# Kernel optimization log

Measured on AMD Instinct MI355X. Metric: run time of the kernel, lower is better.

The kernel has to match this reference:

```python
import jax, jax.numpy as jnp
import numpy as np

B, D, NQ, NK, K = 8, 384, 2048, 2048, 8
NEG_SLOPE = 0.2


def setup_inputs() -> dict:
    key = jax.random.key(0)
    ks = jax.random.split(key, 6)
    return {
        "query_coords": jax.random.normal(ks[0], (B, 3, NQ), jnp.float32),
        "query_features": jax.random.normal(ks[1], (B, D, NQ), jnp.float32),
        "key_coords": jax.random.normal(ks[2], (B, 3, NK), jnp.float32),
        "key_features": jax.random.normal(ks[3], (B, D, NK), jnp.float32),
        "W": jax.random.normal(ks[4], (D, 2 * D), jnp.float32) / np.sqrt(2.0 * D),
        "b": jnp.zeros((D,), jnp.float32),
    }


def _knn_idx(qc, kc, k):
    # qc: [B,3,Nq], kc: [B,3,Nk] -> indices of k nearest keys per query [B,Nq,k]
    q2 = jnp.sum(qc * qc, axis=1)                      # [B,Nq]
    k2 = jnp.sum(kc * kc, axis=1)                      # [B,Nk]
    inner = jnp.einsum('bcq,bck->bqk', qc, kc)         # [B,Nq,Nk]
    dist = q2[:, :, None] - 2.0 * inner + k2[:, None, :]
    _, idx = jax.lax.top_k(-dist, k)
    return idx


def reference(query_coords, query_features, key_coords, key_features, W, b):
    idx = _knn_idx(query_coords, key_coords, K)        # [B,Nq,K]
    kf = jnp.transpose(key_features, (0, 2, 1))        # [B,Nk,D]
    qf = jnp.transpose(query_features, (0, 2, 1))      # [B,Nq,D]
    nbr = jax.vmap(lambda f, i: f[i])(kf, idx)         # gather -> [B,Nq,K,D]
    center = qf[:, :, None, :]                          # [B,Nq,1,D]
    # DGCNN/PoinTr graph feature: concat(neighbor - center, center)
    geom = jnp.concatenate(
        [nbr - center, jnp.broadcast_to(center, nbr.shape)], axis=-1)  # [B,Nq,K,2D]
    h = jnp.einsum('bqkf,df->bqkd', geom, W) + b        # Linear(2D -> D)
    h = jnp.where(h >= 0, h, NEG_SLOPE * h)             # LeakyReLU(0.2)
    return jnp.max(h, axis=2)                           # max over k -> [B,Nq,D]
```

## Files before the change

kernel.cpp:

```cpp
#include <hip/hip_runtime.h>
#include <hip/hip_bf16.h>
#include <float.h>

#define BB 8
#define DD 384
#define NQ 2048
#define NK 2048
#define NEG 0.2f

typedef __attribute__((ext_vector_type(8))) __bf16 bf16x8v;
typedef __attribute__((ext_vector_type(4))) float  float4v;

__device__ __forceinline__ unsigned short bf16_rne(float x) {
  unsigned int u = __float_as_uint(x);
  return (unsigned short)((u + 0x7FFFu + ((u >> 16) & 1u)) >> 16);
}
__device__ __forceinline__ float bf16_to_f32(unsigned short h) {
  return __uint_as_float(((unsigned int)h) << 16);
}

#define QPW 4

__global__ __launch_bounds__(256) void knn_kernel(
    const float* __restrict__ qc, const float* __restrict__ kc,
    int* __restrict__ idx)
{
  __shared__ float4 ksm[NK];
  const int b = blockIdx.y;
  const int t = threadIdx.x;
  const float* kcb = kc + (size_t)b * 3 * NK;
  for (int i = t; i < NK; i += 256) {
    float x = kcb[i], y = kcb[NK + i], z = kcb[2 * NK + i];
    ksm[i] = make_float4(x, y, z, (x * x + y * y) + z * z);
  }
  __syncthreads();

  const int w = t >> 6, l = t & 63;
  const float* qcb = qc + (size_t)b * 3 * NQ;

  for (int qi = 0; qi < QPW; ++qi) {
    const int q = blockIdx.x * (4 * QPW) + w * QPW + qi;
    const float qx = qcb[q], qy = qcb[NQ + q], qz = qcb[2 * NQ + q];
    const float q2 = (qx * qx + qy * qy) + qz * qz;

    float d[32];
    #pragma unroll
    for (int j = 0; j < 32; ++j) {
      float4 kv = ksm[j * 64 + l];
      float inner = (qx * kv.x + qy * kv.y) + qz * kv.z;
      d[j] = (q2 - 2.0f * inner) + kv.w;
    }

    int outk[8];
    #pragma unroll
    for (int r = 0; r < 8; ++r) {
      float m = d[0]; int mj = 0;
      #pragma unroll
      for (int j = 1; j < 32; ++j) {
        bool c = d[j] < m;
        m  = c ? d[j] : m;
        mj = c ? j : mj;
      }
      int mkey = mj * 64 + l;
      #pragma unroll
      for (int off = 32; off >= 1; off >>= 1) {
        float om = __shfl_xor(m, off);
        int   ok = __shfl_xor(mkey, off);
        bool take = (om < m) || (om == m && ok < mkey);
        m    = take ? om : m;
        mkey = take ? ok : mkey;
      }
      outk[r] = mkey;
      const bool mine = (l == (mkey & 63));
      const int  slot = mkey >> 6;
      #pragma unroll
      for (int j = 0; j < 32; ++j) {
        bool kill = mine && (j == slot);
        d[j] = kill ? FLT_MAX : d[j];
      }
    }
    int myv = outk[0];
    #pragma unroll
    for (int r = 1; r < 8; ++r) myv = (l == r) ? outk[r] : myv;
    if (l < 8) idx[((size_t)b * NQ + q) * 8 + l] = myv;
  }
}

__global__ __launch_bounds__(256) void transpose_pack_kernel(
    const float* __restrict__ kf, const float* __restrict__ qf,
    unsigned short* __restrict__ Apk)
{
  __shared__ float tile[64][68];
  const int t = threadIdx.x;
  const int z = blockIdx.z;
  const int b = z & 7;
  const float* src = ((z >> 3) ? qf : kf) + (size_t)b * DD * 2048;
  const int f0 = blockIdx.y * 64;
  const int n0 = blockIdx.x * 64;

  {
    const int fr = t >> 2, nc = (t & 3) * 16;
    const float* p = src + (size_t)(f0 + fr) * 2048 + n0 + nc;
    float4 v0 = *(const float4*)(p);
    float4 v1 = *(const float4*)(p + 4);
    float4 v2 = *(const float4*)(p + 8);
    float4 v3 = *(const float4*)(p + 12);
    *(float4*)&tile[fr][nc]      = v0;
    *(float4*)&tile[fr][nc + 4]  = v1;
    *(float4*)&tile[fr][nc + 8]  = v2;
    *(float4*)&tile[fr][nc + 12] = v3;
  }
  __syncthreads();
  {
    const int nr = t >> 2, fc = (t & 3) * 16;
    unsigned int hp[8], lp[8];
    #pragma unroll
    for (int i = 0; i < 8; ++i) {
      float va = tile[fc + 2 * i][nr];
      float vb = tile[fc + 2 * i + 1][nr];
      unsigned short ha = bf16_rne(va), hb = bf16_rne(vb);
      unsigned short la = bf16_rne(va - bf16_to_f32(ha));
      unsigned short lb = bf16_rne(vb - bf16_to_f32(hb));
      hp[i] = (unsigned int)ha | ((unsigned int)hb << 16);
      lp[i] = (unsigned int)la | ((unsigned int)lb << 16);
    }
    unsigned short* row = Apk + ((size_t)z * 2048 + n0 + nr) * (2 * DD);
    *(uint4*)(row + f0 + fc)          = make_uint4(hp[0], hp[1], hp[2], hp[3]);
    *(uint4*)(row + f0 + fc + 8)      = make_uint4(hp[4], hp[5], hp[6], hp[7]);
    *(uint4*)(row + DD + f0 + fc)     = make_uint4(lp[0], lp[1], lp[2], lp[3]);
    *(uint4*)(row + DD + f0 + fc + 8) = make_uint4(lp[4], lp[5], lp[6], lp[7]);
  }
}

__global__ __launch_bounds__(192) void wpack_kernel(
    const float* __restrict__ W, unsigned short* __restrict__ Wpk)
{
  const int d = blockIdx.x;
  const int mode = blockIdx.y;
  const int t = threadIdx.x;
  const float* wrow = W + (size_t)d * (2 * DD) + t * 2;
  float2 w1 = *(const float2*)(wrow);
  float a = w1.x, c = w1.y;
  if (mode) {
    float2 w2 = *(const float2*)(wrow + DD);
    a = w2.x - a; c = w2.y - c;
  }
  unsigned short ha = bf16_rne(a), hc = bf16_rne(c);
  unsigned short la = bf16_rne(a - bf16_to_f32(ha));
  unsigned short lc = bf16_rne(c - bf16_to_f32(hc));
  unsigned short* orow = Wpk + ((size_t)mode * DD + d) * (2 * DD);
  *(unsigned int*)(orow + t * 2)      = (unsigned int)ha | ((unsigned int)hc << 16);
  *(unsigned int*)(orow + DD + t * 2) = (unsigned int)la | ((unsigned int)lc << 16);
}

__global__ __launch_bounds__(256) void proj_gemm_mfma(
    const unsigned short* __restrict__ Apk,
    const unsigned short* __restrict__ Wpk,
    const float* __restrict__ bias,
    float* __restrict__ pk, float* __restrict__ pq)
{
  __shared__ unsigned short Alds[128][72];
  __shared__ unsigned short Blds[128][72];

  const int t = threadIdx.x;
  const int z = blockIdx.z, b = z & 7, mode = z >> 3;
  const int n0 = blockIdx.x * 128;
  const int d0 = blockIdx.y * 128;
  const int w = t >> 6, l = t & 63;
  const int wn = w & 1, wd = w >> 1;
  const int lr = l & 15, g = l >> 4;

  float4v acc[4][4];
  #pragma unroll
  for (int i = 0; i < 4; ++i)
    #pragma unroll
    for (int j = 0; j < 4; ++j) acc[i][j] = (float4v){0.f, 0.f, 0.f, 0.f};

  const int sr = t >> 1, sh = (t & 1) * 32;
  const unsigned short* asrc = Apk + ((size_t)z * 2048 + n0 + sr) * (2 * DD) + (t & 1) * DD;
  const unsigned short* bsrc = Wpk + ((size_t)mode * DD + d0 + sr) * (2 * DD) + (t & 1) * DD;

  for (int ks = 0; ks < 12; ++ks) {
    const int kt = ks * 32;
    float4 a0 = *(const float4*)(asrc + kt);
    float4 a1 = *(const float4*)(asrc + kt + 8);
    float4 a2 = *(const float4*)(asrc + kt + 16);
    float4 a3 = *(const float4*)(asrc + kt + 24);
    float4 b0 = *(const float4*)(bsrc + kt);
    float4 b1 = *(const float4*)(bsrc + kt + 8);
    float4 b2 = *(const float4*)(bsrc + kt + 16);
    float4 b3 = *(const float4*)(bsrc + kt + 24);
    __syncthreads();
    *(float4*)&Alds[sr][sh]      = a0;
    *(float4*)&Alds[sr][sh + 8]  = a1;
    *(float4*)&Alds[sr][sh + 16] = a2;
    *(float4*)&Alds[sr][sh + 24] = a3;
    *(float4*)&Blds[sr][sh]      = b0;
    *(float4*)&Blds[sr][sh + 8]  = b1;
    *(float4*)&Blds[sr][sh + 16] = b2;
    *(float4*)&Blds[sr][sh + 24] = b3;
    __syncthreads();

    bf16x8v ah[4], al[4], bh[4], bl[4];
    #pragma unroll
    for (int i = 0; i < 4; ++i) {
      ah[i] = *(const bf16x8v*)&Alds[wn * 64 + i * 16 + lr][g * 8];
      al[i] = *(const bf16x8v*)&Alds[wn * 64 + i * 16 + lr][32 + g * 8];
      bh[i] = *(const bf16x8v*)&Blds[wd * 64 + i * 16 + lr][g * 8];
      bl[i] = *(const bf16x8v*)&Blds[wd * 64 + i * 16 + lr][32 + g * 8];
    }
    #pragma unroll
    for (int i = 0; i < 4; ++i)
      #pragma unroll
      for (int j = 0; j < 4; ++j) {
        acc[i][j] = __builtin_amdgcn_mfma_f32_16x16x32_bf16(ah[i], bh[j], acc[i][j], 0, 0, 0);
        acc[i][j] = __builtin_amdgcn_mfma_f32_16x16x32_bf16(ah[i], bl[j], acc[i][j], 0, 0, 0);
        acc[i][j] = __builtin_amdgcn_mfma_f32_16x16x32_bf16(al[i], bh[j], acc[i][j], 0, 0, 0);
      }
  }

  float bv[4];
  #pragma unroll
  for (int j = 0; j < 4; ++j)
    bv[j] = mode ? bias[d0 + wd * 64 + j * 16 + lr] : 0.f;

  float* out = (mode ? pq : pk) + (size_t)b * 2048 * DD;
  #pragma unroll
  for (int i = 0; i < 4; ++i) {
    const int nb_ = n0 + wn * 64 + i * 16 + g * 4;
    #pragma unroll
    for (int j = 0; j < 4; ++j) {
      const int dcol = d0 + wd * 64 + j * 16 + lr;
      #pragma unroll
      for (int r = 0; r < 4; ++r)
        out[(size_t)(nb_ + r) * DD + dcol] = acc[i][j][r] + bv[j];
    }
  }
}

__global__ __launch_bounds__(256) void proj_gemm_all(
    const float* __restrict__ kf, const float* __restrict__ qf,
    const float* __restrict__ W, const float* __restrict__ bias,
    float* __restrict__ pk, float* __restrict__ pq)
{
  __shared__ float At[16][128];
  __shared__ float Bt[16][132];
  const int t = threadIdx.x;
  const int z = blockIdx.z, b = z & 7, mode = z >> 3;
  const int n0 = blockIdx.x * 128, d0 = blockIdx.y * 128;
  const int td = t & 15, tn = t >> 4;
  float acc[8][8];
  #pragma unroll
  for (int i = 0; i < 8; ++i)
    #pragma unroll
    for (int j = 0; j < 8; ++j) acc[i][j] = 0.f;
  const float* feats = mode ? qf : kf;
  float* out = mode ? pq : pk;
  const float* fb = feats + (size_t)b * DD * 2048;
  const int ar = t >> 5, ac = (t & 31) * 4, bdl = t >> 2, bf = (t & 3) * 4;
  float4 sa0, sa1, sw1a, sw1b, sw2a, sw2b;
#define PREFETCH(KT)                                                           \
  {                                                                            \
    sa0 = *(const float4*)&fb[(size_t)((KT) + ar) * 2048 + n0 + ac];           \
    sa1 = *(const float4*)&fb[(size_t)((KT) + ar + 8) * 2048 + n0 + ac];       \
    const float* wr0 = W + (size_t)(d0 + bdl) * (2 * DD) + (KT) + bf;          \
    const float* wr1 = W + (size_t)(d0 + bdl + 64) * (2 * DD) + (KT) + bf;     \
    sw1a = *(const float4*)wr0; sw1b = *(const float4*)wr1;                    \
    if (mode) { sw2a = *(const float4*)(wr0 + DD); sw2b = *(const float4*)(wr1 + DD); } \
  }
  PREFETCH(0);
  for (int kt = 0; kt < DD; kt += 16) {
    *(float4*)&At[ar][ac]     = sa0;
    *(float4*)&At[ar + 8][ac] = sa1;
    {
      float4 w = sw1a;
      if (mode) { w.x = sw2a.x - w.x; w.y = sw2a.y - w.y; w.z = sw2a.z - w.z; w.w = sw2a.w - w.w; }
      Bt[bf + 0][bdl] = w.x; Bt[bf + 1][bdl] = w.y; Bt[bf + 2][bdl] = w.z; Bt[bf + 3][bdl] = w.w;
    }
    {
      float4 w = sw1b;
      if (mode) { w.x = sw2b.x - w.x; w.y = sw2b.y - w.y; w.z = sw2b.z - w.z; w.w = sw2b.w - w.w; }
      Bt[bf + 0][bdl + 64] = w.x; Bt[bf + 1][bdl + 64] = w.y; Bt[bf + 2][bdl + 64] = w.z; Bt[bf + 3][bdl + 64] = w.w;
    }
    __syncthreads();
    if (kt + 16 < DD) PREFETCH(kt + 16);
    #pragma unroll
    for (int k = 0; k < 16; ++k) {
      float a[8], bb[8];
      {
        float4 v = *(const float4*)&At[k][tn * 4];
        a[0] = v.x; a[1] = v.y; a[2] = v.z; a[3] = v.w;
        v = *(const float4*)&At[k][tn * 4 + 64];
        a[4] = v.x; a[5] = v.y; a[6] = v.z; a[7] = v.w;
        v = *(const float4*)&Bt[k][td * 4];
        bb[0] = v.x; bb[1] = v.y; bb[2] = v.z; bb[3] = v.w;
        v = *(const float4*)&Bt[k][td * 4 + 64];
        bb[4] = v.x; bb[5] = v.y; bb[6] = v.z; bb[7] = v.w;
      }
      #pragma unroll
      for (int i = 0; i < 8; ++i)
        #pragma unroll
        for (int j = 0; j < 8; ++j)
          acc[i][j] = fmaf(a[i], bb[j], acc[i][j]);
    }
    __syncthreads();
  }
#undef PREFETCH
  float4 blo = make_float4(0.f, 0.f, 0.f, 0.f);
  float4 bhi = make_float4(0.f, 0.f, 0.f, 0.f);
  if (mode) {
    blo = *(const float4*)&bias[d0 + td * 4];
    bhi = *(const float4*)&bias[d0 + td * 4 + 64];
  }
  float* ob = out + (size_t)b * 2048 * DD;
  #pragma unroll
  for (int i = 0; i < 8; ++i) {
    int n = n0 + tn * 4 + (i & 3) + ((i >= 4) ? 64 : 0);
    float4 c0, c1;
    c0.x = acc[i][0] + blo.x; c0.y = acc[i][1] + blo.y;
    c0.z = acc[i][2] + blo.z; c0.w = acc[i][3] + blo.w;
    c1.x = acc[i][4] + bhi.x; c1.y = acc[i][5] + bhi.y;
    c1.z = acc[i][6] + bhi.z; c1.w = acc[i][7] + bhi.w;
    *(float4*)&ob[(size_t)n * DD + d0 + td * 4]      = c0;
    *(float4*)&ob[(size_t)n * DD + d0 + td * 4 + 64] = c1;
  }
}

__global__ __launch_bounds__(384) void gather_max_kernel(
    const float4* __restrict__ pk4, const float4* pq4,
    const int* __restrict__ idx, float4* out4)
{
  const int t = threadIdx.x;
  const int bq0 = blockIdx.x * 4;
  __shared__ int nb[4][8];
  if (t < 32) nb[t >> 3][t & 7] = idx[(size_t)(bq0 + (t >> 3)) * 8 + (t & 7)];
  __syncthreads();
  const int q_l = t / 96;
  const int dv  = t - q_l * 96;
  const int bq  = bq0 + q_l;
  const int b   = bq >> 11;
  const float4* pkb = pk4 + (size_t)b * NK * 96;
  float4 m = make_float4(-FLT_MAX, -FLT_MAX, -FLT_MAX, -FLT_MAX);
  #pragma unroll
  for (int s = 0; s < 8; ++s) {
    float4 v = pkb[(size_t)nb[q_l][s] * 96 + dv];
    m.x = fmaxf(m.x, v.x); m.y = fmaxf(m.y, v.y);
    m.z = fmaxf(m.z, v.z); m.w = fmaxf(m.w, v.w);
  }
  float4 c = pq4[(size_t)bq * 96 + dv];
  float4 r;
  r.x = m.x + c.x; r.y = m.y + c.y; r.z = m.z + c.z; r.w = m.w + c.w;
  r.x = (r.x >= 0.f) ? r.x : NEG * r.x;
  r.y = (r.y >= 0.f) ? r.y : NEG * r.y;
  r.z = (r.z >= 0.f) ? r.z : NEG * r.z;
  r.w = (r.w >= 0.f) ? r.w : NEG * r.w;
  out4[(size_t)bq * 96 + dv] = r;
}

extern "C" void kernel_launch(void* const* d_in, const int* in_sizes, int n_in,
                              void* d_out, int out_size, void* d_ws, size_t ws_size,
                              hipStream_t stream) {
  const float* qc   = (const float*)d_in[0];
  const float* qf   = (const float*)d_in[1];
  const float* kc   = (const float*)d_in[2];
  const float* kf   = (const float*)d_in[3];
  const float* W    = (const float*)d_in[4];
  const float* bias = (const float*)d_in[5];
  float* out = (float*)d_out;
  char* ws = (char*)d_ws;

  const size_t APK_BYTES = (size_t)16 * 2048 * (2 * DD) * 2;
  const size_t WPK_BYTES = (size_t)2 * DD * (2 * DD) * 2;
  const size_t PK_BYTES  = (size_t)BB * NK * DD * 4;
  const size_t IDX_BYTES = (size_t)BB * NQ * 8 * 4;

  if (ws_size >= APK_BYTES + WPK_BYTES + PK_BYTES + IDX_BYTES) {
    unsigned short* Apk = (unsigned short*)ws;
    unsigned short* Wpk = (unsigned short*)(ws + APK_BYTES);
    float* pk = (float*)(ws + APK_BYTES + WPK_BYTES);
    int*   ix = (int*)  (ws + APK_BYTES + WPK_BYTES + PK_BYTES);
    float* pq = out;

    transpose_pack_kernel<<<dim3(32, 6, 16), 256, 0, stream>>>(kf, qf, Apk);
    wpack_kernel<<<dim3(DD, 2), 192, 0, stream>>>(W, Wpk);
    knn_kernel<<<dim3(NQ / (4 * QPW), BB), 256, 0, stream>>>(qc, kc, ix);
    proj_gemm_mfma<<<dim3(16, 3, 16), 256, 0, stream>>>(Apk, Wpk, bias, pk, pq);
    gather_max_kernel<<<dim3(BB * NQ / 4), 384, 0, stream>>>(
        (const float4*)pk, (const float4*)pq, ix, (float4*)out);
  } else {
    float* pk = (float*)ws;
    float* pq = (float*)(ws + PK_BYTES);
    int*   ix = (int*)  (ws + 2 * PK_BYTES);
    knn_kernel<<<dim3(NQ / (4 * QPW), BB), 256, 0, stream>>>(qc, kc, ix);
    proj_gemm_all<<<dim3(16, 3, 16), 256, 0, stream>>>(kf, qf, W, bias, pk, pq);
    gather_max_kernel<<<dim3(BB * NQ / 4), 384, 0, stream>>>(
        (const float4*)pk, (const float4*)pq, ix, (float4*)out);
  }
}
```

Before: 264.4 us.

## Prepack key coords to global and parallelize KNN with tree argmin

```diff
diff --git a/kernel.cpp b/kernel.cpp
--- a/kernel.cpp
+++ b/kernel.cpp
@@ -19,71 +19,96 @@
   return __uint_as_float(((unsigned int)h) << 16);
 }
 
-#define QPW 4
+__global__ __launch_bounds__(256) void kpack_kernel(
+    const float* __restrict__ kc, float4* __restrict__ kpk)
+{
+  const int b = blockIdx.y;
+  const int i = blockIdx.x * 256 + threadIdx.x;
+  const float* kcb = kc + (size_t)b * 3 * NK;
+  float x = kcb[i], y = kcb[NK + i], z = kcb[2 * NK + i];
+  kpk[(size_t)b * NK + i] = make_float4(x, y, z, (x * x + y * y) + z * z);
+}
 
 __global__ __launch_bounds__(256) void knn_kernel(
-    const float* __restrict__ qc, const float* __restrict__ kc,
+    const float* __restrict__ qc, const float4* __restrict__ kpk,
     int* __restrict__ idx)
 {
-  __shared__ float4 ksm[NK];
+  const int t = threadIdx.x;
   const int b = blockIdx.y;
-  const int t = threadIdx.x;
-  const float* kcb = kc + (size_t)b * 3 * NK;
-  for (int i = t; i < NK; i += 256) {
-    float x = kcb[i], y = kcb[NK + i], z = kcb[2 * NK + i];
-    ksm[i] = make_float4(x, y, z, (x * x + y * y) + z * z);
-  }
-  __syncthreads();
-
   const int w = t >> 6, l = t & 63;
+  const int q = blockIdx.x * 4 + w;
+
   const float* qcb = qc + (size_t)b * 3 * NQ;
-
-  for (int qi = 0; qi < QPW; ++qi) {
-    const int q = blockIdx.x * (4 * QPW) + w * QPW + qi;
-    const float qx = qcb[q], qy = qcb[NQ + q], qz = qcb[2 * NQ + q];
-    const float q2 = (qx * qx + qy * qy) + qz * qz;
-
-    float d[32];
+  const float qx = qcb[q], qy = qcb[NQ + q], qz = qcb[2 * NQ + q];
+  const float q2 = (qx * qx + qy * qy) + qz * qz;
+
+  const float4* kb = kpk + (size_t)b * NK;
+  float d[32];
+  #pragma unroll
+  for (int j = 0; j < 32; ++j) {
+    float4 kv = kb[j * 64 + l];
+    float inner = (qx * kv.x + qy * kv.y) + qz * kv.z;
+    d[j] = (q2 - 2.0f * inner) + kv.w;
+  }
+
+  int outk[8];
+  #pragma unroll
+  for (int r = 0; r < 8; ++r) {
+    float v16[16]; int i16[16];
+    #pragma unroll
+    for (int i = 0; i < 16; ++i) {
+      bool c = d[2 * i + 1] < d[2 * i];
+      v16[i] = c ? d[2 * i + 1] : d[2 * i];
+      i16[i] = c ? 2 * i + 1 : 2 * i;
+    }
+    float v8[8]; int i8[8];
+    #pragma unroll
+    for (int i = 0; i < 8; ++i) {
+      bool c = v16[2 * i + 1] < v16[2 * i];
+      v8[i] = c ? v16[2 * i + 1] : v16[2 * i];
+      i8[i] = c ? i16[2 * i + 1] : i16[2 * i];
+    }
+    float v4[4]; int i4[4];
+    #pragma unroll
+    for (int i = 0; i < 4; ++i) {
+      bool c = v8[2 * i + 1] < v8[2 * i];
+      v4[i] = c ? v8[2 * i + 1] : v8[2 * i];
+      i4[i] = c ? i8[2 * i + 1] : i8[2 * i];
+    }
+    float v2[2]; int i2[2];
+    #pragma unroll
+    for (int i = 0; i < 2; ++i) {
+      bool c = v4[2 * i + 1] < v4[2 * i];
+      v2[i] = c ? v4[2 * i + 1] : v4[2 * i];
+      i2[i] = c ? i4[2 * i + 1] : i4[2 * i];
+    }
+    bool c0 = v2[1] < v2[0];
+    float m = c0 ? v2[1] : v2[0];
+    int  mj = c0 ? i2[1] : i2[0];
+
+    int mkey = mj * 64 + l;
+    #pragma unroll
+    for (int off = 32; off >= 1; off >>= 1) {
+      float om = __shfl_xor(m, off);
+      int   ok = __shfl_xor(mkey, off);
+      bool take = (om < m) || (om == m && ok < mkey);
+      m    = take ? om : m;
+      mkey = take ? ok : mkey;
+    }
+    outk[r] = mkey;
+    const bool mine = (l == (mkey & 63));
+    const int  slot = mkey >> 6;
     #pragma unroll
     for (int j = 0; j < 32; ++j) {
-      float4 kv = ksm[j * 64 + l];
-      float inner = (qx * kv.x + qy * kv.y) + qz * kv.z;
-      d[j] = (q2 - 2.0f * inner) + kv.w;
-    }
-
-    int outk[8];
-    #pragma unroll
-    for (int r = 0; r < 8; ++r) {
-      float m = d[0]; int mj = 0;
-      #pragma unroll
-      for (int j = 1; j < 32; ++j) {
-        bool c = d[j] < m;
-        m  = c ? d[j] : m;
-        mj = c ? j : mj;
-      }
-      int mkey = mj * 64 + l;
-      #pragma unroll
-      for (int off = 32; off >= 1; off >>= 1) {
-        float om = __shfl_xor(m, off);
-        int   ok = __shfl_xor(mkey, off);
-        bool take = (om < m) || (om == m && ok < mkey);
-        m    = take ? om : m;
-        mkey = take ? ok : mkey;
-      }
-      outk[r] = mkey;
-      const bool mine = (l == (mkey & 63));
-      const int  slot = mkey >> 6;
-      #pragma unroll
-      for (int j = 0; j < 32; ++j) {
-        bool kill = mine && (j == slot);
-        d[j] = kill ? FLT_MAX : d[j];
-      }
-    }
-    int myv = outk[0];
-    #pragma unroll
-    for (int r = 1; r < 8; ++r) myv = (l == r) ? outk[r] : myv;
-    if (l < 8) idx[((size_t)b * NQ + q) * 8 + l] = myv;
-  }
+      bool kill = mine && (j == slot);
+      d[j] = kill ? FLT_MAX : d[j];
+    }
+  }
+
+  int myv = outk[0];
+  #pragma unroll
+  for (int r = 1; r < 8; ++r) myv = (l == r) ? outk[r] : myv;
+  if (l < 8) idx[((size_t)b * NQ + q) * 8 + l] = myv;
 }
 
 __global__ __launch_bounds__(256) void transpose_pack_kernel(
@@ -380,10 +405,12 @@
     float* pk = (float*)(ws + APK_BYTES + WPK_BYTES);
     int*   ix = (int*)  (ws + APK_BYTES + WPK_BYTES + PK_BYTES);
     float* pq = out;
-
+    float4* kpk = (float4*)pk;
+
+    kpack_kernel<<<dim3(NK / 256, BB), 256, 0, stream>>>(kc, kpk);
+    knn_kernel<<<dim3(NQ / 4, BB), 256, 0, stream>>>(qc, kpk, ix);
     transpose_pack_kernel<<<dim3(32, 6, 16), 256, 0, stream>>>(kf, qf, Apk);
     wpack_kernel<<<dim3(DD, 2), 192, 0, stream>>>(W, Wpk);
-    knn_kernel<<<dim3(NQ / (4 * QPW), BB), 256, 0, stream>>>(qc, kc, ix);
     proj_gemm_mfma<<<dim3(16, 3, 16), 256, 0, stream>>>(Apk, Wpk, bias, pk, pq);
     gather_max_kernel<<<dim3(BB * NQ / 4), 384, 0, stream>>>(
         (const float4*)pk, (const float4*)pq, ix, (float4*)out);
@@ -391,7 +418,10 @@
     float* pk = (float*)ws;
     float* pq = (float*)(ws + PK_BYTES);
     int*   ix = (int*)  (ws + 2 * PK_BYTES);
-    knn_kernel<<<dim3(NQ / (4 * QPW), BB), 256, 0, stream>>>(qc, kc, ix);
+    float4* kpk = (float4*)pk;
+
+    kpack_kernel<<<dim3(NK / 256, BB), 256, 0, stream>>>(kc, kpk);
+    knn_kernel<<<dim3(NQ / 4, BB), 256, 0, stream>>>(qc, kpk, ix);
     proj_gemm_all<<<dim3(16, 3, 16), 256, 0, stream>>>(kf, qf, W, bias, pk, pq);
     gather_max_kernel<<<dim3(BB * NQ / 4), 384, 0, stream>>>(
         (const float4*)pk, (const float4*)pq, ix, (float4*)out);
```

After: 283.0 us. 7.1% more time.
